# Optimization experiments

Measured on AMD Instinct MI355X. Metric: run time of the kernel, lower is better.

## Reference

```python
import jax, jax.numpy as jnp
import numpy as np

B, T, F, H = 2048, 129, 128, 128  # batch, window, features, hidden


def setup_inputs() -> dict:
    key = jax.random.key(0)
    ks = jax.random.split(key, 7)
    s = 0.05
    return {
        "x": jax.random.normal(ks[0], (B, T - 1, F), jnp.float32),
        "w_lin": jax.random.normal(ks[1], (1, 2 * H + T - 1), jnp.float32) * s,  # attn Linear weight
        "b_lin": jax.random.normal(ks[2], (1,), jnp.float32) * s,
        "w_ih": jax.random.normal(ks[3], (4 * H, F), jnp.float32) * s,  # LSTM input weights (i,f,g,o)
        "w_hh": jax.random.normal(ks[4], (4 * H, H), jnp.float32) * s,
        "b_ih": jax.random.normal(ks[5], (4 * H,), jnp.float32) * s,
        "b_hh": jax.random.normal(ks[6], (4 * H,), jnp.float32) * s,
    }


def _forward(x, w_lin, b_lin, w_ih, w_hh, b_ih, b_hh):
    # x: [B, T-1, F]
    nb, tm1, nf = x.shape
    nh = w_hh.shape[1]
    # Split attention linear weight into the parts applied to h, c, and x-row.
    wh, wc, wx = w_lin[0, :nh], w_lin[0, nh:2 * nh], w_lin[0, 2 * nh:]
    # x.permute(0,2,1) part of the concat is time-invariant: precompute its score.
    s_x = jnp.einsum('btf,t->bf', x, wx)  # [B, F]
    bias = b_ih + b_hh

    def step(carry, xt):
        h, c = carry  # [B, H] each
        # score for feature k = wh.h + wc.c + wx.x[:,k,:] + b  (h/c terms equal for all k)
        scores = (h @ wh + c @ wc + b_lin[0])[:, None] + s_x  # [B, F]
        a = jax.nn.softmax(scores, axis=1)
        xa = a * xt  # attended input at time t, [B, F]
        gates = xa @ w_ih.T + h @ w_hh.T + bias  # [B, 4H]
        i, f, g, o = jnp.split(gates, 4, axis=1)  # torch LSTM gate order
        c_new = jax.nn.sigmoid(f) * c + jax.nn.sigmoid(i) * jnp.tanh(g)
        h_new = jax.nn.sigmoid(o) * jnp.tanh(c_new)
        return (h_new, c_new), (xa, h_new)

    h0 = jnp.zeros((nb, nh), x.dtype)
    _, (xa_seq, h_seq) = jax.lax.scan(step, (h0, h0), x.transpose(1, 0, 2))
    x_atn = xa_seq.transpose(1, 0, 2)  # [B, T-1, F]
    x_enc = h_seq.transpose(1, 0, 2)   # [B, T-1, H]
    return x_atn, x_enc


def reference(x, w_lin, b_lin, w_ih, w_hh, b_ih, b_hh):
    return _forward(x, w_lin, b_lin, w_ih, w_hh, b_ih, b_hh)
```

## Files before the change

### kernel.cpp

```cpp
#include <hip/hip_runtime.h>
#include <hip/hip_bf16.h>

typedef __attribute__((ext_vector_type(8))) short bf16x8;
typedef __attribute__((ext_vector_type(4))) float f32x4;

#define NB 2048
#define TT 128
#define FF 128
#define HH 128
#define NG 512

__device__ __forceinline__ unsigned short f2bf(float x) {
  union { float f; unsigned u; } v; v.f = x;
  unsigned r = (v.u + 0x7fffu + ((v.u >> 16) & 1u)) >> 16;
  return (unsigned short)r;
}
__device__ __forceinline__ unsigned cvtpk_bf16(float lo, float hi) {
  unsigned r;
  asm("v_cvt_pk_bf16_f32 %0, %1, %2" : "=v"(r) : "v"(lo), "v"(hi));
  return r;
}
__device__ __forceinline__ float frcp(float x) { return __builtin_amdgcn_rcpf(x); }
__device__ __forceinline__ float sigf(float x) { return frcp(1.f + __expf(-x)); }
__device__ __forceinline__ float tanh_(float x) {
  float e = __expf(-2.f * x);
  return (1.f - e) * frcp(1.f + e);
}
__device__ __forceinline__ unsigned swzb(int row, int kbyte) {
  return (unsigned)(row * 256 + (kbyte ^ ((row & 7) << 4)));
}
__device__ __forceinline__ void barrier_lds() {
  asm volatile("s_waitcnt lgkmcnt(0)\n\ts_barrier" ::: "memory");
}

__global__ void k_prep(const float* __restrict__ w_ih, const float* __restrict__ w_hh,
                       const float* __restrict__ b_ih, const float* __restrict__ b_hh,
                       unsigned short* __restrict__ wihb, unsigned short* __restrict__ whhb,
                       float* __restrict__ bias) {
  int g = blockIdx.x * blockDim.x + threadIdx.x;
  int gs = gridDim.x * blockDim.x;
  for (int i = g; i < NG * FF; i += gs) {
    wihb[i] = f2bf(w_ih[i]);
    whhb[i] = f2bf(w_hh[i]);
  }
  if (g < NG) bias[g] = b_ih[g] + b_hh[g];
}

__global__ __launch_bounds__(256) void k_attn_xatn(const float* __restrict__ x,
                                                   const float* __restrict__ w_lin,
                                                   float* __restrict__ out) {
  __shared__ float4 red[256];
  __shared__ float wxs[TT];
  __shared__ float4 aSh[32];
  int tid = threadIdx.x;
  int b = blockIdx.x;
  if (tid < TT) wxs[tid] = w_lin[2 * HH + tid];
  __syncthreads();
  const float4* xb4 = (const float4*)(x + (size_t)b * TT * FF);
  float4 xv[16];
  float4 acc = {0.f, 0.f, 0.f, 0.f};
  int tbase = tid >> 5;
#pragma unroll
  for (int k = 0; k < 16; ++k) {
    xv[k] = xb4[tid + k * 256];
    float wt = wxs[tbase + k * 8];
    acc.x += xv[k].x * wt; acc.y += xv[k].y * wt;
    acc.z += xv[k].z * wt; acc.w += xv[k].w * wt;
  }
  red[tid] = acc;
  __syncthreads();
  if (tid < 64) {
    float4 a0 = red[tid], a1 = red[tid + 64], a2 = red[tid + 128], a3 = red[tid + 192];
    a0.x += a1.x + a2.x + a3.x; a0.y += a1.y + a2.y + a3.y;
    a0.z += a1.z + a2.z + a3.z; a0.w += a1.w + a2.w + a3.w;
    red[tid] = a0;
  }
  __syncthreads();
  if (tid < 32) {
    float4 s = red[tid], s2 = red[tid + 32];
    s.x += s2.x; s.y += s2.y; s.z += s2.z; s.w += s2.w;
    float m = fmaxf(fmaxf(s.x, s.y), fmaxf(s.z, s.w));
#pragma unroll
    for (int d = 1; d < 32; d <<= 1) m = fmaxf(m, __shfl_xor(m, d));
    float4 e;
    e.x = __expf(s.x - m); e.y = __expf(s.y - m);
    e.z = __expf(s.z - m); e.w = __expf(s.w - m);
    float sum = e.x + e.y + e.z + e.w;
#pragma unroll
    for (int d = 1; d < 32; d <<= 1) sum += __shfl_xor(sum, d);
    float inv = frcp(sum);
    e.x *= inv; e.y *= inv; e.z *= inv; e.w *= inv;
    aSh[tid] = e;
  }
  __syncthreads();
  float4 av = aSh[tid & 31];
  float4* ob4 = (float4*)(out + (size_t)b * TT * FF);
#pragma unroll
  for (int k = 0; k < 16; ++k) {
    float4 o;
    o.x = xv[k].x * av.x; o.y = xv[k].y * av.y;
    o.z = xv[k].z * av.z; o.w = xv[k].w * av.w;
    ob4[tid + k * 256] = o;
  }
}

__global__ __launch_bounds__(512, 1) void k_rnn_full(const unsigned short* __restrict__ whhb,
                                                     const unsigned short* __restrict__ wihb,
                                                     const float* __restrict__ bias,
                                                     const float* __restrict__ xa,
                                                     float* __restrict__ enc) {
  __shared__ unsigned char hLds[2][2048];
  __shared__ unsigned char xLds[2][2048];
  int tid = threadIdx.x;
  int l = tid & 63, w = tid >> 6;
  int lg = l >> 4;
  bool low = (lg < 2);
  int b0 = blockIdx.x * 8;
  int kl = w * 16 + (l & 15);
  int ar = l & 7;

  bf16x8 Bf[4][8];
  f32x4 bv0, bv1, bv2, bv3;
  {
    float bc0 = bias[0 * 128 + kl], bc1 = bias[1 * 128 + kl];
    float bc2 = bias[2 * 128 + kl], bc3 = bias[3 * 128 + kl];
    bv0 = (f32x4){bc0, bc0, bc0, bc0};
    bv1 = (f32x4){bc1, bc1, bc1, bc1};
    bv2 = (f32x4){bc2, bc2, bc2, bc2};
    bv3 = (f32x4){bc3, bc3, bc3, bc3};
  }
#pragma unroll
  for (int g = 0; g < 4; ++g) {
    int n = g * 128 + kl;
#pragma unroll
    for (int ks = 0; ks < 4; ++ks) {
      Bf[g][ks]     = *(const bf16x8*)(whhb + (size_t)n * HH + ks * 32 + lg * 8);
      Bf[g][4 + ks] = *(const bf16x8*)(wihb + (size_t)n * FF + ks * 32 + lg * 8);
    }
  }
  for (int i = tid; i < 512; i += 512) {
    ((unsigned*)hLds)[i] = 0u; ((unsigned*)hLds)[i + 512] = 0u;
    ((unsigned*)xLds)[i] = 0u; ((unsigned*)xLds)[i + 512] = 0u;
  }
  int srow = tid >> 6, sf = (tid & 63) * 2;
  const float* xrow = xa + (size_t)(b0 + srow) * TT * FF + sf;
  {
    float2 v = *(const float2*)xrow;
    *(unsigned*)(xLds[0] + swzb(srow, sf * 2)) = cvtpk_bf16(v.x, v.y);
  }
  barrier_lds();
  f32x4 xaccA0, xaccA1, xaccA2, xaccA3;
  f32x4 xaccB0, xaccB1, xaccB2, xaccB3;
  float2 pv;
  {
    float2 v = *(const float2*)(xrow + FF);
    bf16x8 Ax[4];
#pragma unroll
    for (int ks = 0; ks < 4; ++ks)
      Ax[ks] = *(const bf16x8*)(xLds[0] + swzb(ar, ks * 64 + lg * 16));
    xaccA0 = bv0; xaccA1 = bv1; xaccA2 = bv2; xaccA3 = bv3;
#pragma unroll
    for (int ks = 0; ks < 4; ++ks) {
      xaccA0 = __builtin_amdgcn_mfma_f32_16x16x32_bf16(Ax[ks], Bf[0][4 + ks], xaccA0, 0, 0, 0);
      xaccA1 = __builtin_amdgcn_mfma_f32_16x16x32_bf16(Ax[ks], Bf[1][4 + ks], xaccA1, 0, 0, 0);
      xaccA2 = __builtin_amdgcn_mfma_f32_16x16x32_bf16(Ax[ks], Bf[2][4 + ks], xaccA2, 0, 0, 0);
      xaccA3 = __builtin_amdgcn_mfma_f32_16x16x32_bf16(Ax[ks], Bf[3][4 + ks], xaccA3, 0, 0, 0);
    }
    *(unsigned*)(xLds[1] + swzb(srow, sf * 2)) = cvtpk_bf16(v.x, v.y);
    pv = *(const float2*)(xrow + 2 * FF);
  }
  barrier_lds();

  int bq0 = ((lg & 1) << 2) | ((lg >> 1) << 1);
  float c0 = 0.f, c1 = 0.f;
  float* pA = enc + (size_t)(b0 + bq0) * TT * HH + kl;
  float* pB = enc + (size_t)(b0 + bq0 + 1) * TT * HH + kl;

#define RNN_BODY(tc, CUR, NXT, XU0, XU1, XU2, XU3, XN0, XN1, XN2, XN3)          \
  {                                                                              \
              \
    *(unsigned*)(xLds[CUR] + swzb(srow, sf * 2)) = cvtpk_bf16(pv.x, pv.y);       \
    pv = *(const float2*)(xrow + (size_t)((tc) + 3) * FF);                       \
    bf16x8 Ah[4], Ax[4];                                                         \
    _Pragma("unroll")                                                            \
    for (int ks = 0; ks < 4; ++ks)                                               \
      Ah[ks] = *(const bf16x8*)(hLds[CUR] + swzb(ar, ks * 64 + lg * 16));        \
    _Pragma("unroll")                                                            \
    for (int ks = 0; ks < 4; ++ks)                                               \
      Ax[ks] = *(const bf16x8*)(xLds[NXT] + swzb(ar, ks * 64 + lg * 16));        \
            \
    f32x4 s0 = XU0, s1 = XU1, s2 = XU2, s3 = XU3;                                \
    _Pragma("unroll")                                                            \
    for (int ks = 0; ks < 4; ++ks) {                                             \
      s0 = __builtin_amdgcn_mfma_f32_16x16x32_bf16(Ah[ks], Bf[0][ks], s0, 0,0,0);\
      s1 = __builtin_amdgcn_mfma_f32_16x16x32_bf16(Ah[ks], Bf[1][ks], s1, 0,0,0);\
      s2 = __builtin_amdgcn_mfma_f32_16x16x32_bf16(Ah[ks], Bf[2][ks], s2, 0,0,0);\
      s3 = __builtin_amdgcn_mfma_f32_16x16x32_bf16(Ah[ks], Bf[3][ks], s3, 0,0,0);\
    }                                                                            \
         \
    XN0 = bv0; XN1 = bv1; XN2 = bv2; XN3 = bv3;                                  \
    _Pragma("unroll")                                                            \
    for (int ks = 0; ks < 4; ++ks) {                                             \
      XN0 = __builtin_amdgcn_mfma_f32_16x16x32_bf16(Ax[ks], Bf[0][4+ks], XN0, 0,0,0);\
      XN1 = __builtin_amdgcn_mfma_f32_16x16x32_bf16(Ax[ks], Bf[1][4+ks], XN1, 0,0,0);\
      XN2 = __builtin_amdgcn_mfma_f32_16x16x32_bf16(Ax[ks], Bf[2][4+ks], XN2, 0,0,0);\
      XN3 = __builtin_amdgcn_mfma_f32_16x16x32_bf16(Ax[ks], Bf[3][4+ks], XN3, 0,0,0);\
    }                                                                            \
    float giA = low ? s0[0] : s0[2], giB = low ? s0[1] : s0[3];                  \
    float gfA = low ? s1[0] : s1[2], gfB = low ? s1[1] : s1[3];                  \
    float ggA = low ? s2[0] : s2[2], ggB = low ? s2[1] : s2[3];                  \
    float goA = low ? s3[0] : s3[2], goB = low ? s3[1] : s3[3];                  \
    float cnA = sigf(gfA) * c0 + sigf(giA) * tanh_(ggA);                         \
    float cnB = sigf(gfB) * c1 + sigf(giB) * tanh_(ggB);                         \
    c0 = cnA; c1 = cnB;                                                          \
    float hvA = sigf(goA) * tanh_(cnA);                                          \
    float hvB = sigf(goB) * tanh_(cnB);                                          \
    unsigned hp = cvtpk_bf16(hvA, hvB);                                          \
    unsigned hq = hp >> 16;                                                      \
    *(unsigned short*)(hLds[NXT] + swzb(bq0, kl * 2)) = (unsigned short)hp;      \
    *(unsigned short*)(hLds[NXT] + swzb(bq0 + 1, kl * 2)) = (unsigned short)hq;  \
    pA[(size_t)(tc) * HH] = hvA;                                                 \
    pB[(size_t)(tc) * HH] = hvB;                                                 \
    barrier_lds();                                                               \
  }

  for (int t = 0; t < TT; t += 2) {
    RNN_BODY(t,     0, 1, xaccA0, xaccA1, xaccA2, xaccA3, xaccB0, xaccB1, xaccB2, xaccB3)
    RNN_BODY(t + 1, 1, 0, xaccB0, xaccB1, xaccB2, xaccB3, xaccA0, xaccA1, xaccA2, xaccA3)
  }
#undef RNN_BODY
}

extern "C" void kernel_launch(void* const* d_in, const int* in_sizes, int n_in,
                              void* d_out, int out_size, void* d_ws, size_t ws_size,
                              hipStream_t stream) {
  (void)in_sizes; (void)n_in; (void)out_size; (void)ws_size;
  const float* x     = (const float*)d_in[0];
  const float* w_lin = (const float*)d_in[1];
  const float* w_ih  = (const float*)d_in[3];
  const float* w_hh  = (const float*)d_in[4];
  const float* b_ih  = (const float*)d_in[5];
  const float* b_hh  = (const float*)d_in[6];
  float* out = (float*)d_out;

  char* ws = (char*)d_ws;
  float* bias          = (float*)ws;
  unsigned short* wihb = (unsigned short*)(ws + 4096);
  unsigned short* whhb = (unsigned short*)(ws + 4096 + (1 << 17));

  float* enc = out + (size_t)NB * TT * FF;

  k_prep<<<dim3(64), dim3(256), 0, stream>>>(w_ih, w_hh, b_ih, b_hh, wihb, whhb, bias);
  k_attn_xatn<<<dim3(NB), dim3(256), 0, stream>>>(x, w_lin, out);
  k_rnn_full<<<dim3(256), dim3(512), 0, stream>>>(whhb, wihb, bias, out, enc);
}
```

Measured before the change: 175.3 us.

## Fuse attention softmax and x_atn computation into the recurrent LSTM kernel

Removes the separate attention kernel and computes each row's time-weighted feature score, softmax, and attended input inside the RNN kernel before the recurrence starts. Each block now reads x directly and writes x_atn on the fly as it streams timesteps, so the RNN no longer re-reads an intermediate xa buffer from global memory and one launch is dropped. In exchange, the RNN kernel first makes a serial pass over all 128 timesteps of x to compute the scores, using only 256 blocks. This could lengthen its critical path compared with the previously wide, 2048-block attention kernel.

```diff
diff --git a/kernel.cpp b/kernel.cpp
--- a/kernel.cpp
+++ b/kernel.cpp
@@ -46,71 +46,16 @@
   if (g < NG) bias[g] = b_ih[g] + b_hh[g];
 }
 
-__global__ __launch_bounds__(256) void k_attn_xatn(const float* __restrict__ x,
-                                                   const float* __restrict__ w_lin,
-                                                   float* __restrict__ out) {
-  __shared__ float4 red[256];
-  __shared__ float wxs[TT];
-  __shared__ float4 aSh[32];
-  int tid = threadIdx.x;
-  int b = blockIdx.x;
-  if (tid < TT) wxs[tid] = w_lin[2 * HH + tid];
-  __syncthreads();
-  const float4* xb4 = (const float4*)(x + (size_t)b * TT * FF);
-  float4 xv[16];
-  float4 acc = {0.f, 0.f, 0.f, 0.f};
-  int tbase = tid >> 5;
-#pragma unroll
-  for (int k = 0; k < 16; ++k) {
-    xv[k] = xb4[tid + k * 256];
-    float wt = wxs[tbase + k * 8];
-    acc.x += xv[k].x * wt; acc.y += xv[k].y * wt;
-    acc.z += xv[k].z * wt; acc.w += xv[k].w * wt;
-  }
-  red[tid] = acc;
-  __syncthreads();
-  if (tid < 64) {
-    float4 a0 = red[tid], a1 = red[tid + 64], a2 = red[tid + 128], a3 = red[tid + 192];
-    a0.x += a1.x + a2.x + a3.x; a0.y += a1.y + a2.y + a3.y;
-    a0.z += a1.z + a2.z + a3.z; a0.w += a1.w + a2.w + a3.w;
-    red[tid] = a0;
-  }
-  __syncthreads();
-  if (tid < 32) {
-    float4 s = red[tid], s2 = red[tid + 32];
-    s.x += s2.x; s.y += s2.y; s.z += s2.z; s.w += s2.w;
-    float m = fmaxf(fmaxf(s.x, s.y), fmaxf(s.z, s.w));
-#pragma unroll
-    for (int d = 1; d < 32; d <<= 1) m = fmaxf(m, __shfl_xor(m, d));
-    float4 e;
-    e.x = __expf(s.x - m); e.y = __expf(s.y - m);
-    e.z = __expf(s.z - m); e.w = __expf(s.w - m);
-    float sum = e.x + e.y + e.z + e.w;
-#pragma unroll
-    for (int d = 1; d < 32; d <<= 1) sum += __shfl_xor(sum, d);
-    float inv = frcp(sum);
-    e.x *= inv; e.y *= inv; e.z *= inv; e.w *= inv;
-    aSh[tid] = e;
-  }
-  __syncthreads();
-  float4 av = aSh[tid & 31];
-  float4* ob4 = (float4*)(out + (size_t)b * TT * FF);
-#pragma unroll
-  for (int k = 0; k < 16; ++k) {
-    float4 o;
-    o.x = xv[k].x * av.x; o.y = xv[k].y * av.y;
-    o.z = xv[k].z * av.z; o.w = xv[k].w * av.w;
-    ob4[tid + k * 256] = o;
-  }
-}
-
-__global__ __launch_bounds__(512, 1) void k_rnn_full(const unsigned short* __restrict__ whhb,
-                                                     const unsigned short* __restrict__ wihb,
-                                                     const float* __restrict__ bias,
-                                                     const float* __restrict__ xa,
-                                                     float* __restrict__ enc) {
+__global__ __launch_bounds__(512, 1) void k_rnn_fused(const unsigned short* __restrict__ whhb,
+                                                      const unsigned short* __restrict__ wihb,
+                                                      const float* __restrict__ bias,
+                                                      const float* __restrict__ x,
+                                                      const float* __restrict__ w_lin,
+                                                      float* __restrict__ xaout_base,
+                                                      float* __restrict__ enc) {
   __shared__ unsigned char hLds[2][2048];
   __shared__ unsigned char xLds[2][2048];
+  __shared__ float wxs[TT];
   int tid = threadIdx.x;
   int l = tid & 63, w = tid >> 6;
   int lg = l >> 4;
@@ -138,22 +83,48 @@
       Bf[g][4 + ks] = *(const bf16x8*)(wihb + (size_t)n * FF + ks * 32 + lg * 8);
     }
   }
-  for (int i = tid; i < 512; i += 512) {
-    ((unsigned*)hLds)[i] = 0u; ((unsigned*)hLds)[i + 512] = 0u;
-    ((unsigned*)xLds)[i] = 0u; ((unsigned*)xLds)[i + 512] = 0u;
-  }
+  if (tid < TT) wxs[tid] = w_lin[2 * HH + tid];
+  ((unsigned*)hLds)[tid] = 0u;
+  ((unsigned*)hLds)[tid + 512] = 0u;
+  __syncthreads();
+
   int srow = tid >> 6, sf = (tid & 63) * 2;
-  const float* xrow = xa + (size_t)(b0 + srow) * TT * FF + sf;
-  {
-    float2 v = *(const float2*)xrow;
-    *(unsigned*)(xLds[0] + swzb(srow, sf * 2)) = cvtpk_bf16(v.x, v.y);
-  }
+  const float* xrow = x + (size_t)(b0 + srow) * TT * FF + sf;
+  float* xaout = xaout_base + (size_t)(b0 + srow) * TT * FF + sf;
+
+  float2 v0p = *(const float2*)(xrow);
+  float2 v1p = *(const float2*)(xrow + FF);
+  float2 v2p = *(const float2*)(xrow + 2 * FF);
+  float s0 = v0p.x * wxs[0] + v1p.x * wxs[1] + v2p.x * wxs[2];
+  float s1 = v0p.y * wxs[0] + v1p.y * wxs[1] + v2p.y * wxs[2];
+#pragma unroll 8
+  for (int t = 3; t < TT; ++t) {
+    float2 v = *(const float2*)(xrow + (size_t)t * FF);
+    s0 += v.x * wxs[t];
+    s1 += v.y * wxs[t];
+  }
+  float m = fmaxf(s0, s1);
+#pragma unroll
+  for (int d = 1; d < 64; d <<= 1) m = fmaxf(m, __shfl_xor(m, d));
+  float e0 = __expf(s0 - m), e1 = __expf(s1 - m);
+  float sum = e0 + e1;
+#pragma unroll
+  for (int d = 1; d < 64; d <<= 1) sum += __shfl_xor(sum, d);
+  float inv = frcp(sum);
+  float a0 = e0 * inv, a1 = e1 * inv;
+
+  float xa00 = v0p.x * a0, xa01 = v0p.y * a1;
+  float xa10 = v1p.x * a0, xa11 = v1p.y * a1;
+  *(float2*)(xaout)      = (float2){xa00, xa01};
+  *(float2*)(xaout + FF) = (float2){xa10, xa11};
+  *(unsigned*)(xLds[0] + swzb(srow, sf * 2)) = cvtpk_bf16(xa00, xa01);
+  *(unsigned*)(xLds[1] + swzb(srow, sf * 2)) = cvtpk_bf16(xa10, xa11);
+  float2 pv = v2p;
   barrier_lds();
+
   f32x4 xaccA0, xaccA1, xaccA2, xaccA3;
   f32x4 xaccB0, xaccB1, xaccB2, xaccB3;
-  float2 pv;
   {
-    float2 v = *(const float2*)(xrow + FF);
     bf16x8 Ax[4];
 #pragma unroll
     for (int ks = 0; ks < 4; ++ks)
@@ -166,8 +137,6 @@
       xaccA2 = __builtin_amdgcn_mfma_f32_16x16x32_bf16(Ax[ks], Bf[2][4 + ks], xaccA2, 0, 0, 0);
       xaccA3 = __builtin_amdgcn_mfma_f32_16x16x32_bf16(Ax[ks], Bf[3][4 + ks], xaccA3, 0, 0, 0);
     }
-    *(unsigned*)(xLds[1] + swzb(srow, sf * 2)) = cvtpk_bf16(v.x, v.y);
-    pv = *(const float2*)(xrow + 2 * FF);
   }
   barrier_lds();
 
@@ -178,9 +147,12 @@
 
 #define RNN_BODY(tc, CUR, NXT, XU0, XU1, XU2, XU3, XN0, XN1, XN2, XN3)          \
   {                                                                              \
-              \
-    *(unsigned*)(xLds[CUR] + swzb(srow, sf * 2)) = cvtpk_bf16(pv.x, pv.y);       \
-    pv = *(const float2*)(xrow + (size_t)((tc) + 3) * FF);                       \
+        \
+    float xv0 = pv.x * a0, xv1 = pv.y * a1;                                      \
+    *(unsigned*)(xLds[CUR] + swzb(srow, sf * 2)) = cvtpk_bf16(xv0, xv1);         \
+    if ((tc) + 2 < TT) *(float2*)(xaout + (size_t)((tc) + 2) * FF) = (float2){xv0, xv1}; \
+    int tnx = ((tc) + 3 < TT) ? (tc) + 3 : TT - 1;                               \
+    pv = *(const float2*)(xrow + (size_t)tnx * FF);                              \
     bf16x8 Ah[4], Ax[4];                                                         \
     _Pragma("unroll")                                                            \
     for (int ks = 0; ks < 4; ++ks)                                               \
@@ -189,13 +161,13 @@
     for (int ks = 0; ks < 4; ++ks)                                               \
       Ax[ks] = *(const bf16x8*)(xLds[NXT] + swzb(ar, ks * 64 + lg * 16));        \
             \
-    f32x4 s0 = XU0, s1 = XU1, s2 = XU2, s3 = XU3;                                \
+    f32x4 s0_ = XU0, s1_ = XU1, s2_ = XU2, s3_ = XU3;                            \
     _Pragma("unroll")                                                            \
     for (int ks = 0; ks < 4; ++ks) {                                             \
-      s0 = __builtin_amdgcn_mfma_f32_16x16x32_bf16(Ah[ks], Bf[0][ks], s0, 0,0,0);\
-      s1 = __builtin_amdgcn_mfma_f32_16x16x32_bf16(Ah[ks], Bf[1][ks], s1, 0,0,0);\
-      s2 = __builtin_amdgcn_mfma_f32_16x16x32_bf16(Ah[ks], Bf[2][ks], s2, 0,0,0);\
-      s3 = __builtin_amdgcn_mfma_f32_16x16x32_bf16(Ah[ks], Bf[3][ks], s3, 0,0,0);\
+      s0_ = __builtin_amdgcn_mfma_f32_16x16x32_bf16(Ah[ks], Bf[0][ks], s0_, 0,0,0);\
+      s1_ = __builtin_amdgcn_mfma_f32_16x16x32_bf16(Ah[ks], Bf[1][ks], s1_, 0,0,0);\
+      s2_ = __builtin_amdgcn_mfma_f32_16x16x32_bf16(Ah[ks], Bf[2][ks], s2_, 0,0,0);\
+      s3_ = __builtin_amdgcn_mfma_f32_16x16x32_bf16(Ah[ks], Bf[3][ks], s3_, 0,0,0);\
     }                                                                            \
          \
     XN0 = bv0; XN1 = bv1; XN2 = bv2; XN3 = bv3;                                  \
@@ -206,10 +178,10 @@
       XN2 = __builtin_amdgcn_mfma_f32_16x16x32_bf16(Ax[ks], Bf[2][4+ks], XN2, 0,0,0);\
       XN3 = __builtin_amdgcn_mfma_f32_16x16x32_bf16(Ax[ks], Bf[3][4+ks], XN3, 0,0,0);\
     }                                                                            \
-    float giA = low ? s0[0] : s0[2], giB = low ? s0[1] : s0[3];                  \
-    float gfA = low ? s1[0] : s1[2], gfB = low ? s1[1] : s1[3];                  \
-    float ggA = low ? s2[0] : s2[2], ggB = low ? s2[1] : s2[3];                  \
-    float goA = low ? s3[0] : s3[2], goB = low ? s3[1] : s3[3];                  \
+    float giA = low ? s0_[0] : s0_[2], giB = low ? s0_[1] : s0_[3];              \
+    float gfA = low ? s1_[0] : s1_[2], gfB = low ? s1_[1] : s1_[3];              \
+    float ggA = low ? s2_[0] : s2_[2], ggB = low ? s2_[1] : s2_[3];              \
+    float goA = low ? s3_[0] : s3_[2], goB = low ? s3_[1] : s3_[3];              \
     float cnA = sigf(gfA) * c0 + sigf(giA) * tanh_(ggA);                         \
     float cnB = sigf(gfB) * c1 + sigf(giB) * tanh_(ggB);                         \
     c0 = cnA; c1 = cnB;                                                          \
@@ -251,6 +223,5 @@
   float* enc = out + (size_t)NB * TT * FF;
 
   k_prep<<<dim3(64), dim3(256), 0, stream>>>(w_ih, w_hh, b_ih, b_hh, wihb, whhb, bias);
-  k_attn_xatn<<<dim3(NB), dim3(256), 0, stream>>>(x, w_lin, out);
-  k_rnn_full<<<dim3(256), dim3(512), 0, stream>>>(whhb, wihb, bias, out, enc);
-}
+  k_rnn_fused<<<dim3(256), dim3(512), 0, stream>>>(whhb, wihb, bias, x, w_lin, out, enc);
+}
```

Result: no change. 178.7 us (+1.9%).
